# Kernel tuning notes

Measured on AMD Instinct MI355X. Metric: run time of the kernel, lower is better.

The kernel has to match this reference:

```python
import jax, jax.numpy as jnp
import numpy as np

B, Q, S, H, D = 4, 1024, 2048, 32, 128  # batch, new tokens, cache capacity, heads, head_dim
SCALE = 0.08838834764831845  # 1/sqrt(128)


def setup_inputs() -> dict:
    key = jax.random.key(0)
    ks = jax.random.split(key, 7)
    query_states = jax.random.normal(ks[0], (B, Q, H, D), jnp.float32)
    key_states = jax.random.normal(ks[1], (B, Q, H, D), jnp.float32)
    value_states = jax.random.normal(ks[2], (B, Q, H, D), jnp.float32)
    k_cache = jax.random.normal(ks[3], (B, S, H, D), jnp.float32)
    v_cache = jax.random.normal(ks[4], (B, S, H, D), jnp.float32)
    q_lens = jax.random.randint(ks[5], (B,), 1, Q + 1).astype(jnp.int32)      # ragged new lengths
    cache_lens = jax.random.randint(ks[6], (B,), 0, Q + 1).astype(jnp.int32)  # prior context lengths
    return dict(query_states=query_states, key_states=key_states, value_states=value_states,
                k_cache=k_cache, v_cache=v_cache, q_lens=q_lens, cache_lens=cache_lens)


def _update_cache(cache, new, cache_lens, q_lens):
    # Per-sequence append: write new[b, :q_len[b]] into cache[b, cache_len[b]:cache_len[b]+q_len[b]]
    def upd(c, n, clen, qlen):
        j = jnp.arange(Q)
        idx = jnp.clip(clen + j, 0, S - 1)               # [Q]
        valid = j < qlen                                  # [Q]
        vals = jnp.where(valid[:, None, None], n, c[idx])  # keep old value where padded
        return c.at[idx].set(vals)
    return jax.vmap(upd)(cache, new, cache_lens, q_lens)


def reference(query_states, key_states, value_states, k_cache, v_cache, q_lens, cache_lens):
    kc = _update_cache(k_cache, key_states, cache_lens, q_lens)   # [B,S,H,D]
    vc = _update_cache(v_cache, value_states, cache_lens, q_lens)

    scores = jnp.einsum('bqhd,bkhd->bhqk', query_states, kc) * SCALE  # [B,H,Q,S]

    qi = jnp.arange(Q)
    kj = jnp.arange(S)
    # query i may attend to cache pos j iff j < cache_len + min(i+1, q_len)  (causal + segment bound)
    limit = cache_lens[:, None] + jnp.minimum(qi[None, :] + 1, q_lens[:, None])  # [B,Q]
    mask = kj[None, None, :] < limit[:, :, None]                                  # [B,Q,S]
    scores = jnp.where(mask[:, None, :, :], scores, -jnp.inf)
    probs = jax.nn.softmax(scores, axis=-1)

    out = jnp.einsum('bhqk,bkhd->bqhd', probs, vc)  # [B,Q,H,D]
    q_valid = (qi[None, :] < q_lens[:, None])[:, :, None, None]
    return jnp.where(q_valid, out, jnp.zeros((), out.dtype))
```

## Files before the change

kernel.cpp:

```cpp
#include <hip/hip_runtime.h>


#define BB 4
#define QQ 1024
#define SS 2048
#define HH 32
#define DD 128
#define QT 64
#define KT 32
#define NTILES 64
#define TILE_ELEMS 4096
#define NPERQ 256

typedef __attribute__((ext_vector_type(8))) short short8;
typedef __attribute__((ext_vector_type(4))) float f32x4;
typedef __attribute__((ext_vector_type(16))) float f32x16;
typedef __attribute__((ext_vector_type(4))) unsigned int u32x4;
typedef __attribute__((ext_vector_type(8))) unsigned short u16x8;

__device__ __forceinline__ unsigned short f2bf(float f) {
    unsigned int u = __builtin_bit_cast(unsigned int, f);
    u += 0x7FFFu + ((u >> 16) & 1u);
    return (unsigned short)(u >> 16);
}
__device__ __forceinline__ unsigned int cvtpk(float lo, float hi) {
    unsigned int r;
    asm("v_cvt_pk_bf16_f32 %0, %1, %2" : "=v"(r) : "v"(lo), "v"(hi));
    return r;
}
__device__ __forceinline__ void glds16(const unsigned short* g, unsigned short* l) {
    __builtin_amdgcn_global_load_lds(
        (const __attribute__((address_space(1))) unsigned int*)g,
        (__attribute__((address_space(3))) unsigned int*)l, 16, 0, 0);
}

__global__ __launch_bounds__(256)
void prep(const float* __restrict__ ks, const float* __restrict__ vs,
          const float* __restrict__ kc_, const float* __restrict__ vc,
          const int* __restrict__ qlens, const int* __restrict__ clens,
          unsigned short* __restrict__ Kws, unsigned short* __restrict__ Vws)
{
    const int tile = blockIdx.x, h = blockIdx.y, b = blockIdx.z;
    const int qlen = qlens[b], clen = clens[b];
    if (tile * KT >= clen + qlen) return;
    const int tid = threadIdx.x;
    unsigned short* kout = Kws + (((size_t)b * HH + h) * NTILES + tile) * TILE_ELEMS;
    unsigned short* vout = Vws + (((size_t)b * HH + h) * NTILES + tile) * TILE_ELEMS;

    #pragma unroll
    for (int h2 = 0; h2 < 2; ++h2) {
        const int idx8 = h2 * 2048 + tid * 8;
        const int c = idx8 >> 9, l = (idx8 >> 3) & 63;
        int key = tile * KT + (l & 31);
        const float* src;
        if (key < clen) {
            src = kc_ + (((size_t)b * SS + key) * HH + h) * DD;
        } else {
            int i2 = key - clen; if (i2 > QQ - 1) i2 = QQ - 1;
            src = ks + (((size_t)b * QQ + i2) * HH + h) * DD;
        }
        const int d0 = c * 16 + ((l >> 5) << 3);
        f32x4 a0 = *(const f32x4*)&src[d0];
        f32x4 a1 = *(const f32x4*)&src[d0 + 4];
        u16x8 w;
        w[0] = f2bf(a0[0]); w[1] = f2bf(a0[1]); w[2] = f2bf(a0[2]); w[3] = f2bf(a0[3]);
        w[4] = f2bf(a1[0]); w[5] = f2bf(a1[1]); w[6] = f2bf(a1[2]); w[7] = f2bf(a1[3]);
        *(u16x8*)&kout[idx8] = w;
    }
    #pragma unroll
    for (int h2 = 0; h2 < 2; ++h2) {
        const int idx8 = h2 * 2048 + tid * 8;
        const int a = idx8 >> 9, l = (idx8 >> 3) & 63;
        const int dchunk = a >> 1, kcc = a & 1;
        const int d = dchunk * 32 + (l & 31);
        const int kb = tile * KT + kcc * 16 + ((l >> 5) << 3);
        u16x8 w;
        #pragma unroll
        for (int e = 0; e < 8; ++e) {
            int key = kb + e;
            const float* src;
            if (key < clen) {
                src = vc + (((size_t)b * SS + key) * HH + h) * DD;
            } else {
                int i2 = key - clen; if (i2 > QQ - 1) i2 = QQ - 1;
                src = vs + (((size_t)b * QQ + i2) * HH + h) * DD;
            }
            w[e] = f2bf(src[d]);
        }
        *(u16x8*)&vout[idx8] = w;
    }
}

__global__ __launch_bounds__(128, 2)
void segattn_persist(const float* __restrict__ qs, const int* __restrict__ qlens,
                     const int* __restrict__ clens,
                     const unsigned short* __restrict__ Kws,
                     const unsigned short* __restrict__ Vws,
                     float* __restrict__ out, int* __restrict__ counter)
{
    __shared__ int s_item;
    alignas(16) __shared__ unsigned short KVl[2][8192];

    const int tid = threadIdx.x, w = tid >> 6, lane = tid & 63;
    const int q31 = lane & 31, hi = lane >> 5;
    const bool hiL = (hi != 0);
    const float psc = 0.08838834764831845f * 1.4426950408889634f;
    const int sbase = w * 2048 + lane * 8;
    const int lbase = w * 2048;
    const int cres = blockIdx.x & 7;
    int* myctr = counter + cres;

    for (;;) {
        if (tid == 0) s_item = atomicAdd(myctr, 1);
        __syncthreads();
        const int pop = s_item;
        __syncthreads();
        if (pop >= NPERQ) break;

        const int bhi = pop >> 4, qtord = pop & 15;
        const int qt = 15 - qtord;
        const int b = bhi & 3, h = cres + 8 * (bhi >> 2);
        const int qlen = qlens[b], clen = clens[b];
        const int q0 = qt * QT;

        if (q0 >= qlen) {
            f32x4 z = {0.f, 0.f, 0.f, 0.f};
            #pragma unroll
            for (int i2 = 0; i2 < 16; ++i2) {
                int f = tid + i2 * 128;
                int r = f >> 5, d4 = f & 31;
                *(f32x4*)&out[(((size_t)b * QQ + q0 + r) * HH + h) * DD + d4 * 4] = z;
            }
            continue;
        }

        const int q = q0 + w * 32 + q31;
        const float* qp = qs + (((size_t)b * QQ + q) * HH + h) * DD;
        short8 qf[8];
        #pragma unroll
        for (int c = 0; c < 8; ++c) {
            const int d0 = c * 16 + hi * 8;
            f32x4 a0 = *(const f32x4*)&qp[d0];
            f32x4 a1 = *(const f32x4*)&qp[d0 + 4];
            short8 t;
            t[0] = (short)f2bf(a0[0] * psc); t[1] = (short)f2bf(a0[1] * psc);
            t[2] = (short)f2bf(a0[2] * psc); t[3] = (short)f2bf(a0[3] * psc);
            t[4] = (short)f2bf(a1[0] * psc); t[5] = (short)f2bf(a1[1] * psc);
            t[6] = (short)f2bf(a1[2] * psc); t[7] = (short)f2bf(a1[3] * psc);
            qf[c] = t;
        }

        const int lim_l = (q < qlen) ? (clen + q + 1) : 0;
        const int wq0 = q0 + w * 32;
        const int lim_min = (wq0 + 31 < qlen) ? (clen + wq0 + 1) : 0;

        float m_ = -3e38f, l_ = 0.f;
        f32x16 o0 = {0}, o1 = {0}, o2 = {0}, o3 = {0};

        const int kmax = clen + min(q0 + QT, qlen);
        const int nt = (kmax + KT - 1) / KT;
        const unsigned short* Kb = Kws + ((size_t)(b * HH + h)) * NTILES * TILE_ELEMS;
        const unsigned short* Vb = Vws + ((size_t)(b * HH + h)) * NTILES * TILE_ELEMS;

        #pragma unroll
        for (int j = 0; j < 4; ++j) {
            glds16(&Kb[sbase + j * 512], &KVl[0][lbase + j * 512]);
            glds16(&Vb[sbase + j * 512], &KVl[0][4096 + lbase + j * 512]);
        }
        asm volatile("s_waitcnt vmcnt(0)" ::: "memory");
        __builtin_amdgcn_s_barrier();
        __builtin_amdgcn_sched_barrier(0);

        int cur = 0;
        for (int t = 0; t < nt; ++t) {
            const int nb = cur ^ 1;
            const int tnx = (t + 1 < nt) ? t + 1 : (nt - 1);
            const unsigned short* ktn = Kb + (size_t)tnx * TILE_ELEMS;
            const unsigned short* vtn = Vb + (size_t)tnx * TILE_ELEMS;
            #pragma unroll
            for (int j = 0; j < 4; ++j) {
                glds16(&ktn[sbase + j * 512], &KVl[nb][lbase + j * 512]);
                glds16(&vtn[sbase + j * 512], &KVl[nb][4096 + lbase + j * 512]);
            }

            const unsigned short* Kc = &KVl[cur][0];
            const int pbase = t * KT;
            f32x16 s = {0};
            __builtin_amdgcn_s_setprio(1);
            #pragma unroll
            for (int c = 0; c < 8; ++c) {
                short8 kf = *(const short8*)&Kc[c * 512 + lane * 8];
                s = __builtin_amdgcn_mfma_f32_32x32x16_bf16(kf, qf[c], s, 0, 0, 0);
            }
            __builtin_amdgcn_s_setprio(0);
            if (pbase + KT > lim_min) {
                #pragma unroll
                for (int r = 0; r < 16; ++r) {
                    const int kk = pbase + (r & 3) + ((r >> 2) << 3) + hi * 4;
                    if (kk >= lim_l) s[r] = -3e38f;
                }
            }
            float pm = fmaxf(fmaxf(fmaxf(fmaxf(s[0], s[1]), fmaxf(s[2], s[3])),
                                   fmaxf(fmaxf(s[4], s[5]), fmaxf(s[6], s[7]))),
                             fmaxf(fmaxf(fmaxf(s[8], s[9]), fmaxf(s[10], s[11])),
                                   fmaxf(fmaxf(s[12], s[13]), fmaxf(s[14], s[15]))));
            if (__any(pm > m_ + 8.0f)) {
                pm = fmaxf(pm, __shfl_xor(pm, 32));
                const float mn = fmaxf(m_, pm);
                const float alpha = __builtin_amdgcn_exp2f(m_ - mn);
                m_ = mn;
                l_ *= alpha;
                #pragma unroll
                for (int r = 0; r < 16; ++r) {
                    o0[r] *= alpha; o1[r] *= alpha; o2[r] *= alpha; o3[r] *= alpha;
                }
            }
            float p[16];
            #pragma unroll
            for (int r = 0; r < 16; ++r) p[r] = __builtin_amdgcn_exp2f(s[r] - m_);
            l_ += (((p[0]+p[1])+(p[2]+p[3])) + ((p[4]+p[5])+(p[6]+p[7])))
                + (((p[8]+p[9])+(p[10]+p[11])) + ((p[12]+p[13])+(p[14]+p[15])));

            const unsigned int w0 = cvtpk(p[0],  p[1]);
            const unsigned int w1 = cvtpk(p[2],  p[3]);
            const unsigned int w2 = cvtpk(p[4],  p[5]);
            const unsigned int w3 = cvtpk(p[6],  p[7]);
            const unsigned int w4 = cvtpk(p[8],  p[9]);
            const unsigned int w5 = cvtpk(p[10], p[11]);
            const unsigned int w6 = cvtpk(p[12], p[13]);
            const unsigned int w7 = cvtpk(p[14], p[15]);
            const unsigned int x0 = (unsigned int)__shfl_xor((int)w0, 32);
            const unsigned int x1 = (unsigned int)__shfl_xor((int)w1, 32);
            const unsigned int x2 = (unsigned int)__shfl_xor((int)w2, 32);
            const unsigned int x3 = (unsigned int)__shfl_xor((int)w3, 32);
            const unsigned int x4 = (unsigned int)__shfl_xor((int)w4, 32);
            const unsigned int x5 = (unsigned int)__shfl_xor((int)w5, 32);
            const unsigned int x6 = (unsigned int)__shfl_xor((int)w6, 32);
            const unsigned int x7 = (unsigned int)__shfl_xor((int)w7, 32);
            u32x4 pb0w, pb1w;
            pb0w[0] = hiL ? x2 : w0;  pb0w[1] = hiL ? x3 : w1;
            pb0w[2] = hiL ? w2 : x0;  pb0w[3] = hiL ? w3 : x1;
            pb1w[0] = hiL ? x6 : w4;  pb1w[1] = hiL ? x7 : w5;
            pb1w[2] = hiL ? w6 : x4;  pb1w[3] = hiL ? w7 : x5;
            const short8 pb0 = __builtin_bit_cast(short8, pb0w);
            const short8 pb1 = __builtin_bit_cast(short8, pb1w);

            __builtin_amdgcn_s_setprio(1);
            {
                short8 va = *(const short8*)&Kc[4096 + 0 * 512 + lane * 8];
                short8 vb = *(const short8*)&Kc[4096 + 1 * 512 + lane * 8];
                o0 = __builtin_amdgcn_mfma_f32_32x32x16_bf16(va, pb0, o0, 0, 0, 0);
                o0 = __builtin_amdgcn_mfma_f32_32x32x16_bf16(vb, pb1, o0, 0, 0, 0);
            }
            {
                short8 va = *(const short8*)&Kc[4096 + 2 * 512 + lane * 8];
                short8 vb = *(const short8*)&Kc[4096 + 3 * 512 + lane * 8];
                o1 = __builtin_amdgcn_mfma_f32_32x32x16_bf16(va, pb0, o1, 0, 0, 0);
                o1 = __builtin_amdgcn_mfma_f32_32x32x16_bf16(vb, pb1, o1, 0, 0, 0);
            }
            {
                short8 va = *(const short8*)&Kc[4096 + 4 * 512 + lane * 8];
                short8 vb = *(const short8*)&Kc[4096 + 5 * 512 + lane * 8];
                o2 = __builtin_amdgcn_mfma_f32_32x32x16_bf16(va, pb0, o2, 0, 0, 0);
                o2 = __builtin_amdgcn_mfma_f32_32x32x16_bf16(vb, pb1, o2, 0, 0, 0);
            }
            {
                short8 va = *(const short8*)&Kc[4096 + 6 * 512 + lane * 8];
                short8 vb = *(const short8*)&Kc[4096 + 7 * 512 + lane * 8];
                o3 = __builtin_amdgcn_mfma_f32_32x32x16_bf16(va, pb0, o3, 0, 0, 0);
                o3 = __builtin_amdgcn_mfma_f32_32x32x16_bf16(vb, pb1, o3, 0, 0, 0);
            }
            __builtin_amdgcn_s_setprio(0);

            asm volatile("s_waitcnt vmcnt(0)" ::: "memory");
            __builtin_amdgcn_s_barrier();
            __builtin_amdgcn_sched_barrier(0);
            cur = nb;
        }

        float lt = l_ + __shfl_xor(l_, 32);
        const bool val = (q < qlen);
        const float inv = val ? (1.0f / lt) : 0.f;
        float* op = out + (((size_t)b * QQ + q) * HH + h) * DD;
        #pragma unroll
        for (int rr = 0; rr < 4; ++rr) {
            f32x4 wv;
            const int d0 = rr * 8 + hi * 4;
            wv[0] = o0[rr*4+0]*inv; wv[1] = o0[rr*4+1]*inv;
            wv[2] = o0[rr*4+2]*inv; wv[3] = o0[rr*4+3]*inv;
            *(f32x4*)&op[d0] = wv;
            wv[0] = o1[rr*4+0]*inv; wv[1] = o1[rr*4+1]*inv;
            wv[2] = o1[rr*4+2]*inv; wv[3] = o1[rr*4+3]*inv;
            *(f32x4*)&op[32 + d0] = wv;
            wv[0] = o2[rr*4+0]*inv; wv[1] = o2[rr*4+1]*inv;
            wv[2] = o2[rr*4+2]*inv; wv[3] = o2[rr*4+3]*inv;
            *(f32x4*)&op[64 + d0] = wv;
            wv[0] = o3[rr*4+0]*inv; wv[1] = o3[rr*4+1]*inv;
            wv[2] = o3[rr*4+2]*inv; wv[3] = o3[rr*4+3]*inv;
            *(f32x4*)&op[96 + d0] = wv;
        }
    }
}

__global__ __launch_bounds__(256)
void segattn(const float* __restrict__ qs, const float* __restrict__ ks,
             const float* __restrict__ vs, const float* __restrict__ kc,
             const float* __restrict__ vc, const int* __restrict__ qlens,
             const int* __restrict__ clens, float* __restrict__ out)
{
    const int qt = blockIdx.x, h = blockIdx.y, b = blockIdx.z;
    const int tid = threadIdx.x, wave = tid >> 6, lane = tid & 63;
    const int g = lane >> 4, lc = lane & 15;
    const int qlen = qlens[b], clen = clens[b];
    const int q0 = qt * QT;
    if (q0 >= qlen) {
        f32x4 z = {0.f, 0.f, 0.f, 0.f};
        #pragma unroll
        for (int i2 = 0; i2 < 8; ++i2) {
            int f = tid + i2 * 256;
            int r = f >> 5, d4 = f & 31;
            *(f32x4*)&out[(((size_t)b * QQ + q0 + r) * HH + h) * DD + d4 * 4] = z;
        }
        return;
    }
    alignas(16) __shared__ unsigned short Kl[KT * DD];
    alignas(16) __shared__ unsigned short Vl[DD * 40];
    alignas(16) __shared__ unsigned short Pl[4][16][40];
    const float psc = 0.08838834764831845f * 1.4426950408889634f;
    const int qrow = q0 + wave * 16 + lc;
    const float* qp = qs + (((size_t)b * QQ + qrow) * HH + h) * DD;
    short8 qf[4];
    #pragma unroll
    for (int c = 0; c < 4; ++c) {
        f32x4 a0 = *(const f32x4*)&qp[c * 32 + g * 8];
        f32x4 a1 = *(const f32x4*)&qp[c * 32 + g * 8 + 4];
        short8 t;
        t[0] = (short)f2bf(a0[0] * psc); t[1] = (short)f2bf(a0[1] * psc);
        t[2] = (short)f2bf(a0[2] * psc); t[3] = (short)f2bf(a0[3] * psc);
        t[4] = (short)f2bf(a1[0] * psc); t[5] = (short)f2bf(a1[1] * psc);
        t[6] = (short)f2bf(a1[2] * psc); t[7] = (short)f2bf(a1[3] * psc);
        qf[c] = t;
    }
    f32x4 o[8];
    #pragma unroll
    for (int n = 0; n < 8; ++n) o[n] = (f32x4){0.f, 0.f, 0.f, 0.f};
    float m_[4] = {-3e38f, -3e38f, -3e38f, -3e38f};
    float l_[4] = {0.f, 0.f, 0.f, 0.f};
    int lim[4];
    #pragma unroll
    for (int qq = 0; qq < 4; ++qq) {
        int i = q0 + wave * 16 + g * 4 + qq;
        lim[qq] = (i < qlen) ? (clen + i + 1) : 0;
    }
    const int kmax = clen + min(q0 + QT, qlen);
    const int nt = (kmax + KT - 1) / KT;
    for (int t = 0; t < nt; ++t) {
        const int pbase = t * KT;
        __syncthreads();
        #pragma unroll
        for (int it = 0; it < 4; ++it) {
            int f = tid + it * 256;
            int key = f >> 5, d4 = f & 31;
            int p = pbase + key;
            const float *srck, *srcv;
            if (p < clen) {
                size_t off = (((size_t)b * SS + p) * HH + h) * DD + d4 * 4;
                srck = kc + off; srcv = vc + off;
            } else {
                int idx = p - clen; if (idx > QQ - 1) idx = QQ - 1;
                size_t off = (((size_t)b * QQ + idx) * HH + h) * DD + d4 * 4;
                srck = ks + off; srcv = vs + off;
            }
            f32x4 kv = *(const f32x4*)srck;
            f32x4 vv = *(const f32x4*)srcv;
            int ei = (key * DD + d4 * 4) ^ ((key & 7) << 3);
            typedef __attribute__((ext_vector_type(4))) unsigned short u16x4;
            u16x4 kb4 = {f2bf(kv[0]), f2bf(kv[1]), f2bf(kv[2]), f2bf(kv[3])};
            *(u16x4*)&Kl[ei] = kb4;
            int d0 = d4 * 4;
            Vl[(d0 + 0) * 40 + key] = f2bf(vv[0]);
            Vl[(d0 + 1) * 40 + key] = f2bf(vv[1]);
            Vl[(d0 + 2) * 40 + key] = f2bf(vv[2]);
            Vl[(d0 + 3) * 40 + key] = f2bf(vv[3]);
        }
        __syncthreads();
        f32x4 sc0 = {0.f, 0.f, 0.f, 0.f}, sc1 = {0.f, 0.f, 0.f, 0.f};
        #pragma unroll
        for (int c = 0; c < 4; ++c) {
            int i0 = (lc * DD + c * 32 + g * 8) ^ ((lc & 7) << 3);
            int i1 = ((16 + lc) * DD + c * 32 + g * 8) ^ (((16 + lc) & 7) << 3);
            short8 k0 = *(const short8*)&Kl[i0];
            short8 k1 = *(const short8*)&Kl[i1];
            sc0 = __builtin_amdgcn_mfma_f32_16x16x32_bf16(qf[c], k0, sc0, 0, 0, 0);
            sc1 = __builtin_amdgcn_mfma_f32_16x16x32_bf16(qf[c], k1, sc1, 0, 0, 0);
        }
        float pr0[4], pr1[4];
        #pragma unroll
        for (int qq = 0; qq < 4; ++qq) {
            float s0 = sc0[qq], s1 = sc1[qq];
            if (pbase + lc >= lim[qq])      s0 = -3e38f;
            if (pbase + 16 + lc >= lim[qq]) s1 = -3e38f;
            float pm = fmaxf(s0, s1);
            #pragma unroll
            for (int d2 = 1; d2 < 16; d2 <<= 1) pm = fmaxf(pm, __shfl_xor(pm, d2));
            float mn = fmaxf(m_[qq], pm);
            float alpha = exp2f(m_[qq] - mn);
            float p0 = exp2f(s0 - mn), p1 = exp2f(s1 - mn);
            float rs = p0 + p1;
            #pragma unroll
            for (int d2 = 1; d2 < 16; d2 <<= 1) rs += __shfl_xor(rs, d2);
            l_[qq] = l_[qq] * alpha + rs;
            m_[qq] = mn;
            pr0[qq] = p0; pr1[qq] = p1;
            #pragma unroll
            for (int n = 0; n < 8; ++n) o[n][qq] *= alpha;
        }
        #pragma unroll
        for (int qq = 0; qq < 4; ++qq) {
            Pl[wave][g * 4 + qq][lc]      = f2bf(pr0[qq]);
            Pl[wave][g * 4 + qq][16 + lc] = f2bf(pr1[qq]);
        }
        short8 pf = *(const short8*)&Pl[wave][lc][g * 8];
        #pragma unroll
        for (int n = 0; n < 8; ++n) {
            short8 vf = *(const short8*)&Vl[(n * 16 + lc) * 40 + g * 8];
            o[n] = __builtin_amdgcn_mfma_f32_16x16x32_bf16(pf, vf, o[n], 0, 0, 0);
        }
    }
    #pragma unroll
    for (int qq = 0; qq < 4; ++qq) {
        int i = q0 + wave * 16 + g * 4 + qq;
        bool val = (i < qlen);
        float inv = val ? (1.0f / l_[qq]) : 0.f;
        size_t ob = (((size_t)b * QQ + i) * HH + h) * DD + lc;
        #pragma unroll
        for (int n = 0; n < 8; ++n)
            out[ob + (size_t)n * 16] = val ? o[n][qq] * inv : 0.f;
    }
}

extern "C" void kernel_launch(void* const* d_in, const int* in_sizes, int n_in,
                              void* d_out, int out_size, void* d_ws, size_t ws_size,
                              hipStream_t stream) {
    const float* qs = (const float*)d_in[0];
    const float* ks = (const float*)d_in[1];
    const float* vs = (const float*)d_in[2];
    const float* kc = (const float*)d_in[3];
    const float* vc = (const float*)d_in[4];
    const int* ql = (const int*)d_in[5];
    const int* cl = (const int*)d_in[6];
    float* o = (float*)d_out;

    const size_t kv_elems = (size_t)BB * HH * NTILES * TILE_ELEMS;
    const size_t kv_bytes = kv_elems * 2 * sizeof(unsigned short);
    const size_t need = kv_bytes + 128;

    if (ws_size >= need) {
        unsigned short* Kws = (unsigned short*)d_ws;
        unsigned short* Vws = Kws + kv_elems;
        int* counter = (int*)((char*)d_ws + kv_bytes);
        hipMemsetAsync(counter, 0, 128, stream);
        dim3 pgrid(NTILES, HH, BB), pblk(256, 1, 1);
        hipLaunchKernelGGL(prep, pgrid, pblk, 0, stream, ks, vs, kc, vc, ql, cl, Kws, Vws);
        dim3 grid(1024, 1, 1), blk(128, 1, 1);
        hipLaunchKernelGGL(segattn_persist, grid, blk, 0, stream, qs, ql, cl, Kws, Vws, o, counter);
    } else {
        dim3 grid(QQ / QT, HH, BB), blk(256, 1, 1);
        hipLaunchKernelGGL(segattn, grid, blk, 0, stream, qs, ks, vs, kc, vc, ql, cl, o);
    }
}
```

Measured before the change: 173.6 us.

## Software-pipeline QK^T of next tile with softmax and PV of current tile

Restructures the attention inner loop so the QK^T MFMAs for tile t+1 are issued together with the PV MFMAs for tile t, after the softmax of tile t. The loop is unrolled by two with ping-pong score registers, and the global-to-LDS prefetch is moved to after the second barrier, targeting tile t+2. The aim is to overlap the exp/shuffle softmax work with matrix-core work and to keep the MFMA pipe busier. It adds an extra barrier per tile and more live registers, which could hurt occupancy under the 128-thread, 2-blocks launch bounds.

Measured after the change: 156.5 us. 1.11x faster.

```diff
diff --git a/kernel.cpp b/kernel.cpp
--- a/kernel.cpp
+++ b/kernel.cpp
@@ -91,6 +91,107 @@
     }
 }
 
+#define TSTEP(T, SC, SN, BC, BN)                                                \
+{                                                                               \
+    const int pbase = (T) * KT;                                                 \
+    if (pbase + KT > lim_min) {                                                 \
+        _Pragma("unroll")                                                       \
+        for (int r = 0; r < 16; ++r) {                                          \
+            const int kk = pbase + (r & 3) + ((r >> 2) << 3) + hi * 4;          \
+            if (kk >= lim_l) SC[r] = -3e38f;                                    \
+        }                                                                       \
+    }                                                                           \
+    float pm = fmaxf(fmaxf(fmaxf(fmaxf(SC[0], SC[1]), fmaxf(SC[2], SC[3])),     \
+                           fmaxf(fmaxf(SC[4], SC[5]), fmaxf(SC[6], SC[7]))),    \
+                     fmaxf(fmaxf(fmaxf(SC[8], SC[9]), fmaxf(SC[10], SC[11])),   \
+                           fmaxf(fmaxf(SC[12], SC[13]), fmaxf(SC[14], SC[15])))); \
+    if (__any(pm > m_ + 8.0f)) {                                                \
+        pm = fmaxf(pm, __shfl_xor(pm, 32));                                     \
+        const float mn = fmaxf(m_, pm);                                         \
+        const float alpha = __builtin_amdgcn_exp2f(m_ - mn);                    \
+        m_ = mn;                                                                \
+        l_ *= alpha;                                                            \
+        _Pragma("unroll")                                                       \
+        for (int r = 0; r < 16; ++r) {                                          \
+            o0[r] *= alpha; o1[r] *= alpha; o2[r] *= alpha; o3[r] *= alpha;     \
+        }                                                                       \
+    }                                                                           \
+    float p[16];                                                                \
+    _Pragma("unroll")                                                           \
+    for (int r = 0; r < 16; ++r) p[r] = __builtin_amdgcn_exp2f(SC[r] - m_);     \
+    l_ += (((p[0]+p[1])+(p[2]+p[3])) + ((p[4]+p[5])+(p[6]+p[7])))               \
+        + (((p[8]+p[9])+(p[10]+p[11])) + ((p[12]+p[13])+(p[14]+p[15])));        \
+    const unsigned int w0 = cvtpk(p[0],  p[1]);                                 \
+    const unsigned int w1 = cvtpk(p[2],  p[3]);                                 \
+    const unsigned int w2 = cvtpk(p[4],  p[5]);                                 \
+    const unsigned int w3 = cvtpk(p[6],  p[7]);                                 \
+    const unsigned int w4 = cvtpk(p[8],  p[9]);                                 \
+    const unsigned int w5 = cvtpk(p[10], p[11]);                                \
+    const unsigned int w6 = cvtpk(p[12], p[13]);                                \
+    const unsigned int w7 = cvtpk(p[14], p[15]);                                \
+    const unsigned int x0 = (unsigned int)__shfl_xor((int)w0, 32);              \
+    const unsigned int x1 = (unsigned int)__shfl_xor((int)w1, 32);              \
+    const unsigned int x2 = (unsigned int)__shfl_xor((int)w2, 32);              \
+    const unsigned int x3 = (unsigned int)__shfl_xor((int)w3, 32);              \
+    const unsigned int x4 = (unsigned int)__shfl_xor((int)w4, 32);              \
+    const unsigned int x5 = (unsigned int)__shfl_xor((int)w5, 32);              \
+    const unsigned int x6 = (unsigned int)__shfl_xor((int)w6, 32);              \
+    const unsigned int x7 = (unsigned int)__shfl_xor((int)w7, 32);              \
+    u32x4 pb0w, pb1w;                                                           \
+    pb0w[0] = hiL ? x2 : w0;  pb0w[1] = hiL ? x3 : w1;                          \
+    pb0w[2] = hiL ? w2 : x0;  pb0w[3] = hiL ? w3 : x1;                          \
+    pb1w[0] = hiL ? x6 : w4;  pb1w[1] = hiL ? x7 : w5;                          \
+    pb1w[2] = hiL ? w6 : x4;  pb1w[3] = hiL ? w7 : x5;                          \
+    const short8 pb0 = __builtin_bit_cast(short8, pb0w);                        \
+    const short8 pb1 = __builtin_bit_cast(short8, pb1w);                        \
+    asm volatile("s_waitcnt vmcnt(0)" ::: "memory");                            \
+    __builtin_amdgcn_s_barrier();                                               \
+    __builtin_amdgcn_sched_barrier(0);                                          \
+    SN = (f32x16){0.f};                                                         \
+    __builtin_amdgcn_s_setprio(1);                                              \
+    _Pragma("unroll")                                                           \
+    for (int c = 0; c < 8; ++c) {                                               \
+        short8 kf = *(const short8*)&KVl[BN][c * 512 + lane * 8];               \
+        SN = __builtin_amdgcn_mfma_f32_32x32x16_bf16(kf, qf[c], SN, 0, 0, 0);   \
+    }                                                                           \
+    {                                                                           \
+        short8 va = *(const short8*)&KVl[BC][4096 + 0 * 512 + lane * 8];        \
+        short8 vb = *(const short8*)&KVl[BC][4096 + 1 * 512 + lane * 8];        \
+        o0 = __builtin_amdgcn_mfma_f32_32x32x16_bf16(va, pb0, o0, 0, 0, 0);     \
+        o0 = __builtin_amdgcn_mfma_f32_32x32x16_bf16(vb, pb1, o0, 0, 0, 0);     \
+    }                                                                           \
+    {                                                                           \
+        short8 va = *(const short8*)&KVl[BC][4096 + 2 * 512 + lane * 8];        \
+        short8 vb = *(const short8*)&KVl[BC][4096 + 3 * 512 + lane * 8];        \
+        o1 = __builtin_amdgcn_mfma_f32_32x32x16_bf16(va, pb0, o1, 0, 0, 0);     \
+        o1 = __builtin_amdgcn_mfma_f32_32x32x16_bf16(vb, pb1, o1, 0, 0, 0);     \
+    }                                                                           \
+    {                                                                           \
+        short8 va = *(const short8*)&KVl[BC][4096 + 4 * 512 + lane * 8];        \
+        short8 vb = *(const short8*)&KVl[BC][4096 + 5 * 512 + lane * 8];        \
+        o2 = __builtin_amdgcn_mfma_f32_32x32x16_bf16(va, pb0, o2, 0, 0, 0);     \
+        o2 = __builtin_amdgcn_mfma_f32_32x32x16_bf16(vb, pb1, o2, 0, 0, 0);     \
+    }                                                                           \
+    {                                                                           \
+        short8 va = *(const short8*)&KVl[BC][4096 + 6 * 512 + lane * 8];        \
+        short8 vb = *(const short8*)&KVl[BC][4096 + 7 * 512 + lane * 8];        \
+        o3 = __builtin_amdgcn_mfma_f32_32x32x16_bf16(va, pb0, o3, 0, 0, 0);     \
+        o3 = __builtin_amdgcn_mfma_f32_32x32x16_bf16(vb, pb1, o3, 0, 0, 0);     \
+    }                                                                           \
+    __builtin_amdgcn_s_setprio(0);                                              \
+    asm volatile("s_waitcnt lgkmcnt(0)" ::: "memory");                          \
+    __builtin_amdgcn_s_barrier();                                               \
+    __builtin_amdgcn_sched_barrier(0);                                          \
+    const int t2c = ((T) + 2 < nt) ? (T) + 2 : (nt - 1);                        \
+    const unsigned short* k2p = Kb + (size_t)t2c * TILE_ELEMS;                  \
+    const unsigned short* v2p = Vb + (size_t)t2c * TILE_ELEMS;                  \
+    _Pragma("unroll")                                                           \
+    for (int j = 0; j < 4; ++j) {                                               \
+        glds16(&k2p[sbase + j * 512], &KVl[BC][lbase + j * 512]);               \
+        glds16(&v2p[sbase + j * 512], &KVl[BC][4096 + lbase + j * 512]);        \
+    }                                                                           \
+}
+
 __global__ __launch_bounds__(128, 2)
 void segattn_persist(const float* __restrict__ qs, const int* __restrict__ qlens,
                      const int* __restrict__ clens,
@@ -170,112 +271,32 @@
         asm volatile("s_waitcnt vmcnt(0)" ::: "memory");
         __builtin_amdgcn_s_barrier();
         __builtin_amdgcn_sched_barrier(0);
-
-        int cur = 0;
-        for (int t = 0; t < nt; ++t) {
-            const int nb = cur ^ 1;
-            const int tnx = (t + 1 < nt) ? t + 1 : (nt - 1);
-            const unsigned short* ktn = Kb + (size_t)tnx * TILE_ELEMS;
-            const unsigned short* vtn = Vb + (size_t)tnx * TILE_ELEMS;
+        {
+            const int t1x = (nt > 1) ? 1 : 0;
+            const unsigned short* k1p = Kb + (size_t)t1x * TILE_ELEMS;
+            const unsigned short* v1p = Vb + (size_t)t1x * TILE_ELEMS;
             #pragma unroll
             for (int j = 0; j < 4; ++j) {
-                glds16(&ktn[sbase + j * 512], &KVl[nb][lbase + j * 512]);
-                glds16(&vtn[sbase + j * 512], &KVl[nb][4096 + lbase + j * 512]);
+                glds16(&k1p[sbase + j * 512], &KVl[1][lbase + j * 512]);
+                glds16(&v1p[sbase + j * 512], &KVl[1][4096 + lbase + j * 512]);
             }
-
-            const unsigned short* Kc = &KVl[cur][0];
-            const int pbase = t * KT;
-            f32x16 s = {0};
-            __builtin_amdgcn_s_setprio(1);
-            #pragma unroll
-            for (int c = 0; c < 8; ++c) {
-                short8 kf = *(const short8*)&Kc[c * 512 + lane * 8];
-                s = __builtin_amdgcn_mfma_f32_32x32x16_bf16(kf, qf[c], s, 0, 0, 0);
-            }
-            __builtin_amdgcn_s_setprio(0);
-            if (pbase + KT > lim_min) {
-                #pragma unroll
-                for (int r = 0; r < 16; ++r) {
-                    const int kk = pbase + (r & 3) + ((r >> 2) << 3) + hi * 4;
-                    if (kk >= lim_l) s[r] = -3e38f;
-                }
-            }
-            float pm = fmaxf(fmaxf(fmaxf(fmaxf(s[0], s[1]), fmaxf(s[2], s[3])),
-                                   fmaxf(fmaxf(s[4], s[5]), fmaxf(s[6], s[7]))),
-                             fmaxf(fmaxf(fmaxf(s[8], s[9]), fmaxf(s[10], s[11])),
-                                   fmaxf(fmaxf(s[12], s[13]), fmaxf(s[14], s[15]))));
-            if (__any(pm > m_ + 8.0f)) {
-                pm = fmaxf(pm, __shfl_xor(pm, 32));
-                const float mn = fmaxf(m_, pm);
-                const float alpha = __builtin_amdgcn_exp2f(m_ - mn);
-                m_ = mn;
-                l_ *= alpha;
-                #pragma unroll
-                for (int r = 0; r < 16; ++r) {
-                    o0[r] *= alpha; o1[r] *= alpha; o2[r] *= alpha; o3[r] *= alpha;
-                }
-            }
-            float p[16];
-            #pragma unroll
-            for (int r = 0; r < 16; ++r) p[r] = __builtin_amdgcn_exp2f(s[r] - m_);
-            l_ += (((p[0]+p[1])+(p[2]+p[3])) + ((p[4]+p[5])+(p[6]+p[7])))
-                + (((p[8]+p[9])+(p[10]+p[11])) + ((p[12]+p[13])+(p[14]+p[15])));
-
-            const unsigned int w0 = cvtpk(p[0],  p[1]);
-            const unsigned int w1 = cvtpk(p[2],  p[3]);
-            const unsigned int w2 = cvtpk(p[4],  p[5]);
-            const unsigned int w3 = cvtpk(p[6],  p[7]);
-            const unsigned int w4 = cvtpk(p[8],  p[9]);
-            const unsigned int w5 = cvtpk(p[10], p[11]);
-            const unsigned int w6 = cvtpk(p[12], p[13]);
-            const unsigned int w7 = cvtpk(p[14], p[15]);
-            const unsigned int x0 = (unsigned int)__shfl_xor((int)w0, 32);
-            const unsigned int x1 = (unsigned int)__shfl_xor((int)w1, 32);
-            const unsigned int x2 = (unsigned int)__shfl_xor((int)w2, 32);
-            const unsigned int x3 = (unsigned int)__shfl_xor((int)w3, 32);
-            const unsigned int x4 = (unsigned int)__shfl_xor((int)w4, 32);
-            const unsigned int x5 = (unsigned int)__shfl_xor((int)w5, 32);
-            const unsigned int x6 = (unsigned int)__shfl_xor((int)w6, 32);
-            const unsigned int x7 = (unsigned int)__shfl_xor((int)w7, 32);
-            u32x4 pb0w, pb1w;
-            pb0w[0] = hiL ? x2 : w0;  pb0w[1] = hiL ? x3 : w1;
-            pb0w[2] = hiL ? w2 : x0;  pb0w[3] = hiL ? w3 : x1;
-            pb1w[0] = hiL ? x6 : w4;  pb1w[1] = hiL ? x7 : w5;
-            pb1w[2] = hiL ? w6 : x4;  pb1w[3] = hiL ? w7 : x5;
-            const short8 pb0 = __builtin_bit_cast(short8, pb0w);
-            const short8 pb1 = __builtin_bit_cast(short8, pb1w);
-
-            __builtin_amdgcn_s_setprio(1);
-            {
-                short8 va = *(const short8*)&Kc[4096 + 0 * 512 + lane * 8];
-                short8 vb = *(const short8*)&Kc[4096 + 1 * 512 + lane * 8];
-                o0 = __builtin_amdgcn_mfma_f32_32x32x16_bf16(va, pb0, o0, 0, 0, 0);
-                o0 = __builtin_amdgcn_mfma_f32_32x32x16_bf16(vb, pb1, o0, 0, 0, 0);
-            }
-            {
-                short8 va = *(const short8*)&Kc[4096 + 2 * 512 + lane * 8];
-                short8 vb = *(const short8*)&Kc[4096 + 3 * 512 + lane * 8];
-                o1 = __builtin_amdgcn_mfma_f32_32x32x16_bf16(va, pb0, o1, 0, 0, 0);
-                o1 = __builtin_amdgcn_mfma_f32_32x32x16_bf16(vb, pb1, o1, 0, 0, 0);
-            }
-            {
-                short8 va = *(const short8*)&Kc[4096 + 4 * 512 + lane * 8];
-                short8 vb = *(const short8*)&Kc[4096 + 5 * 512 + lane * 8];
-                o2 = __builtin_amdgcn_mfma_f32_32x32x16_bf16(va, pb0, o2, 0, 0, 0);
-                o2 = __builtin_amdgcn_mfma_f32_32x32x16_bf16(vb, pb1, o2, 0, 0, 0);
-            }
-            {
-                short8 va = *(const short8*)&Kc[4096 + 6 * 512 + lane * 8];
-                short8 vb = *(const short8*)&Kc[4096 + 7 * 512 + lane * 8];
-                o3 = __builtin_amdgcn_mfma_f32_32x32x16_bf16(va, pb0, o3, 0, 0, 0);
-                o3 = __builtin_amdgcn_mfma_f32_32x32x16_bf16(vb, pb1, o3, 0, 0, 0);
-            }
-            __builtin_amdgcn_s_setprio(0);
-
-            asm volatile("s_waitcnt vmcnt(0)" ::: "memory");
-            __builtin_amdgcn_s_barrier();
-            __builtin_amdgcn_sched_barrier(0);
-            cur = nb;
+        }
+        f32x16 sA = {0}, sB;
+        __builtin_amdgcn_s_setprio(1);
+        #pragma unroll
+        for (int c = 0; c < 8; ++c) {
+            short8 kf = *(const short8*)&KVl[0][c * 512 + lane * 8];
+            sA = __builtin_amdgcn_mfma_f32_32x32x16_bf16(kf, qf[c], sA, 0, 0, 0);
+        }
+        __builtin_amdgcn_s_setprio(0);
+
+        int t = 0;
+        for (; t + 2 <= nt; t += 2) {
+            TSTEP(t,     sA, sB, 0, 1);
+            TSTEP(t + 1, sB, sA, 1, 0);
+        }
+        if (t < nt) {
+            TSTEP(t, sA, sB, 0, 1);
         }
 
         float lt = l_ + __shfl_xor(l_, 32);
```
